# Kernel tuning notes

Hardware: AMD Instinct MI355X
Metric: run time of the kernel (lower is better)

The kernel has to match this reference:

```python
import jax, jax.numpy as jnp
import numpy as np

V, D, B, L = 100000, 64, 4096, 200

def setup_inputs() -> dict:
    key = jax.random.key(0)
    ks = jax.random.split(key, 10)
    s = 0.05  # keep activations in a sane range for sigmoid
    return {
        "item_ids": jax.random.randint(ks[0], (B,), 0, V),
        "history": jax.random.randint(ks[1], (B, L), 0, V),
        "hist_len": jax.random.randint(ks[2], (B,), 1, L + 1),
        "emb_table": jax.random.normal(ks[3], (V, D), jnp.float32) * s,
        "aW1": jax.random.normal(ks[4], (3 * D, D), jnp.float32) * s,
        "ab1": jnp.zeros((D,), jnp.float32),
        "aW2": jax.random.normal(ks[5], (D, 1), jnp.float32) * s,
        "ab2": jnp.zeros((1,), jnp.float32),
        "fW1": jax.random.normal(ks[6], (3 * D, 128), jnp.float32) * s,
        "fb1": jnp.zeros((128,), jnp.float32),
        "fW2": jax.random.normal(ks[7], (128, 64), jnp.float32) * s,
        "fb2": jnp.zeros((64,), jnp.float32),
        "fW3": jax.random.normal(ks[8], (64, 1), jnp.float32) * s,
        "fb3": jnp.zeros((1,), jnp.float32),
    }

def reference(item_ids, history, hist_len, emb_table, aW1, ab1, aW2, ab2,
              fW1, fb1, fW2, fb2, fW3, fb3):
    target = emb_table[item_ids]                      # [B, D]
    hist = emb_table[history]                         # [B, L, D]
    # original pads short histories with zero rows -> zero the padded tail
    mask = (jnp.arange(hist.shape[1])[None, :] < hist_len[:, None]).astype(hist.dtype)
    hist = hist * mask[..., None]
    tgt = jnp.broadcast_to(target[:, None, :], hist.shape)     # [B, L, D]
    # attention_fc takes 3*D features: (hist, target, hist*target)
    feat = jnp.concatenate([hist, tgt, hist * tgt], axis=-1)   # [B, L, 3D]
    h = jax.nn.relu(feat @ aW1 + ab1)                 # [B, L, D]
    scores = (h @ aW2 + ab2)[..., 0]                  # [B, L]
    # faithful to original: softmax over full padded length (no length mask)
    w = jax.nn.softmax(scores, axis=1)
    pooled = jnp.einsum('bl,bld->bd', w, hist)        # [B, D]
    comb = jnp.concatenate([target, pooled, pooled - target], axis=-1)  # [B, 3D]
    z = jax.nn.relu(comb @ fW1 + fb1)
    z = jax.nn.relu(z @ fW2 + fb2)
    return jax.nn.sigmoid(z @ fW3 + fb3)              # [B, 1]
```

## Files before the change

kernel.cpp:

```cpp
#include <hip/hip_runtime.h>
#include <hip/hip_bf16.h>

#define NV 100000
#define ND 64
#define NB 4096
#define NL 200
#define MT 13

typedef __bf16 bf16_t;
typedef __bf16 bf16x8 __attribute__((ext_vector_type(8)));
typedef float f32x4 __attribute__((ext_vector_type(4)));

#define TB_ELEMS ((long)NV * ND)
#define FW1_ELEMS (192 * 128)
#define FW2_ELEMS (128 * 64)
#define CVT_TOTAL (TB_ELEMS + FW1_ELEMS + FW2_ELEMS)

__global__ __launch_bounds__(256)
void cvt_kernel(const float* __restrict__ emb,
                const float* __restrict__ fW1,
                const float* __restrict__ fW2,
                bf16_t* __restrict__ tb)
{
    long i = ((long)blockIdx.x * 256 + threadIdx.x) * 8;
    if (i >= CVT_TOTAL) return;
    const float* src;
    if (i < TB_ELEMS)                  src = emb + i;
    else if (i < TB_ELEMS + FW1_ELEMS) src = fW1 + (i - TB_ELEMS);
    else                               src = fW2 + (i - TB_ELEMS - FW1_ELEMS);
    f32x4 a0 = *(const f32x4*)(src);
    f32x4 a1 = *(const f32x4*)(src + 4);
    bf16x8 o;
#pragma unroll
    for (int j = 0; j < 4; ++j) { o[j] = (bf16_t)a0[j]; o[j + 4] = (bf16_t)a1[j]; }
    *(bf16x8*)(tb + i) = o;
}

__global__ __launch_bounds__(512, 4)
void din_kernel1(const int* __restrict__ item_ids,
                 const int* __restrict__ history,
                 const int* __restrict__ hist_len,
                 const float* __restrict__ emb,
                 const bf16_t* __restrict__ tb,
                 const float* __restrict__ aW1,
                 const float* __restrict__ ab1,
                 const float* __restrict__ aW2,
                 const bf16_t* __restrict__ fW1b, const float* __restrict__ fb1,
                 const bf16_t* __restrict__ fW2b, const float* __restrict__ fb2,
                 const float* __restrict__ fW3, const float* __restrict__ fb3,
                 float* __restrict__ out)
{
    __shared__ __align__(16) bf16_t histA[2][208 * 64];
    __shared__ __align__(16) bf16_t wbT[2][64 * 64];
    __shared__ float tgt[2][64];
    __shared__ __align__(16) float scores[2][208];
    __shared__ float wts[2][208];
    __shared__ float pp2[2][512];
    __shared__ float red[2][8];

    float* pp7 = (float*)histA;
    float* z1  = (float*)histA + 8192;
    float* z2  = (float*)histA + 8448;

    const int b0  = blockIdx.x * 2;
    const int tid = threadIdx.x;
    const int len0 = hist_len[b0];
    const int len1 = hist_len[b0 + 1];

    if (tid < 128) {
        int bx = tid >> 6, d = tid & 63;
        tgt[bx][d] = emb[(long)item_ids[b0 + bx] * ND + d];
    }

    {
        const int p = tid & 1;
        const int s = tid >> 1;
        const int bxA = (s >= 208);
        const int lA  = s - bxA * 208;
        const int lB  = s + 48;
        const int lenA = bxA ? len1 : len0;
        const bool vB = (s < 160);
        const bf16x8 z = (bf16x8)(bf16_t)0.f;
        bf16x8 a0 = z, a1 = z, a2 = z, a3 = z;
        bf16x8 c0 = z, c1 = z, c2 = z, c3 = z;
        if (lA < lenA) {
            const bf16_t* src = tb + (long)history[(long)(b0 + bxA) * NL + lA] * ND + p * 32;
            a0 = *(const bf16x8*)(src);
            a1 = *(const bf16x8*)(src + 8);
            a2 = *(const bf16x8*)(src + 16);
            a3 = *(const bf16x8*)(src + 24);
        }
        if (vB && lB < len1) {
            const bf16_t* src = tb + (long)history[(long)(b0 + 1) * NL + lB] * ND + p * 32;
            c0 = *(const bf16x8*)(src);
            c1 = *(const bf16x8*)(src + 8);
            c2 = *(const bf16x8*)(src + 16);
            c3 = *(const bf16x8*)(src + 24);
        }
        {
            bf16_t* d = &histA[bxA][lA * 64];
            const int S = (lA & 7) << 3;
            *(bf16x8*)&d[(p * 32 +  0) ^ S] = a0;
            *(bf16x8*)&d[(p * 32 +  8) ^ S] = a1;
            *(bf16x8*)&d[(p * 32 + 16) ^ S] = a2;
            *(bf16x8*)&d[(p * 32 + 24) ^ S] = a3;
        }
        if (vB) {
            bf16_t* d = &histA[1][lB * 64];
            const int S = (lB & 7) << 3;
            *(bf16x8*)&d[(p * 32 +  0) ^ S] = c0;
            *(bf16x8*)&d[(p * 32 +  8) ^ S] = c1;
            *(bf16x8*)&d[(p * 32 + 16) ^ S] = c2;
            *(bf16x8*)&d[(p * 32 + 24) ^ S] = c3;
        }
    }

    {
        const int n  = tid & 63;
        const int kp = tid >> 6;
        const long t0 = (long)item_ids[b0] * ND;
        const long t1 = (long)item_ids[b0 + 1] * ND;
        f32x4 tk0a = *(const f32x4*)(emb + t0 + kp * 8);
        f32x4 tk0b = *(const f32x4*)(emb + t0 + kp * 8 + 4);
        f32x4 tk1a = *(const f32x4*)(emb + t1 + kp * 8);
        f32x4 tk1b = *(const f32x4*)(emb + t1 + kp * 8 + 4);
        float cs0 = 0.f, cs1 = 0.f;
        bf16x8 w0v, w1v;
#pragma unroll
        for (int i = 0; i < 8; ++i) {
            int k = kp * 8 + i;
            float tk0 = (i < 4) ? tk0a[i] : tk0b[i - 4];
            float tk1 = (i < 4) ? tk1a[i] : tk1b[i - 4];
            float ah = aW1[k * 64 + n];
            float am = aW1[(64 + k) * 64 + n];
            float ap = aW1[(128 + k) * 64 + n];
            w0v[i] = (bf16_t)(ah + tk0 * ap);
            w1v[i] = (bf16_t)(ah + tk1 * ap);
            cs0 += tk0 * am;
            cs1 += tk1 * am;
        }
        const int S = (n & 7) << 3;
        *(bf16x8*)&wbT[0][n * 64 + ((kp * 8) ^ S)] = w0v;
        *(bf16x8*)&wbT[1][n * 64 + ((kp * 8) ^ S)] = w1v;
        pp2[0][kp * 64 + n] = cs0;
        pp2[1][kp * 64 + n] = cs1;
    }
    __syncthreads();

    {
        const int wave = tid >> 6;
        const int lane = tid & 63;
        const int bx   = wave & 1;
        const int col  = lane & 15;
        const int quad = lane >> 4;

        bf16x8 bfrag[4][2];
#pragma unroll
        for (int nt = 0; nt < 4; ++nt) {
            const int n = nt * 16 + col;
            const int S = (n & 7) << 3;
#pragma unroll
            for (int kb = 0; kb < 2; ++kb)
                bfrag[nt][kb] = *(const bf16x8*)&wbT[bx][n * 64 + ((kb * 32 + quad * 8) ^ S)];
        }
        float cvals[4], a2vals[4];
#pragma unroll
        for (int nt = 0; nt < 4; ++nt) {
            const int n = nt * 16 + col;
            float s = ab1[n];
#pragma unroll
            for (int kp = 0; kp < 8; ++kp) s += pp2[bx][kp * 64 + n];
            cvals[nt]  = s;
            a2vals[nt] = aW2[n];
        }

        for (int mt = (wave >> 1); mt < MT; mt += 4) {
            const int row = mt * 16 + col;
            const int S   = (row & 7) << 3;
            const bf16_t* base = &histA[bx][row * 64];
            bf16x8 af0 = *(const bf16x8*)&base[(     quad * 8) ^ S];
            bf16x8 af1 = *(const bf16x8*)&base[(32 + quad * 8) ^ S];
            float sc[4] = {0.f, 0.f, 0.f, 0.f};
#pragma unroll
            for (int nt = 0; nt < 4; ++nt) {
                f32x4 acc = {0.f, 0.f, 0.f, 0.f};
                acc = __builtin_amdgcn_mfma_f32_16x16x32_bf16(af0, bfrag[nt][0], acc, 0, 0, 0);
                acc = __builtin_amdgcn_mfma_f32_16x16x32_bf16(af1, bfrag[nt][1], acc, 0, 0, 0);
#pragma unroll
                for (int i = 0; i < 4; ++i) {
                    float h = acc[i] + cvals[nt];
                    h = h > 0.f ? h : 0.f;
                    sc[i] += h * a2vals[nt];
                }
            }
            for (int off = 1; off < 16; off <<= 1)
#pragma unroll
                for (int i = 0; i < 4; ++i)
                    sc[i] += __shfl_xor(sc[i], off, 64);
            if (col == 0) {
                f32x4 outv = {sc[0], sc[1], sc[2], sc[3]};
                *(f32x4*)&scores[bx][mt * 16 + quad * 4] = outv;
            }
        }
    }
    __syncthreads();

    {
        const int bx = tid >> 8, t = tid & 255;
        float s = (t < NL) ? scores[bx][t] : -1e30f;
        float m = s;
        for (int off = 32; off > 0; off >>= 1) m = fmaxf(m, __shfl_xor(m, off, 64));
        if ((t & 63) == 0) red[bx][t >> 6] = m;
        __syncthreads();
        m = fmaxf(fmaxf(red[bx][0], red[bx][1]), fmaxf(red[bx][2], red[bx][3]));
        float e = (t < NL) ? __expf(s - m) : 0.f;
        if (t < NL) wts[bx][t] = e;
        float ss = e;
        for (int off = 32; off > 0; off >>= 1) ss += __shfl_xor(ss, off, 64);
        if ((t & 63) == 0) red[bx][4 + (t >> 6)] = ss;
        __syncthreads();
    }

    {
        const int wave = tid >> 6, lane = tid & 63;
        const int bx = wave >> 2, q = wave & 3;
        const float rtot = 1.f / (red[bx][4] + red[bx][5] + red[bx][6] + red[bx][7]);
        float acc = 0.f;
        for (int i = 0; i < 50; ++i) {
            int l = q * 50 + i;
            acc += wts[bx][l] * (float)histA[bx][l * 64 + (lane ^ ((l & 7) << 3))];
        }
        pp2[bx][q * 64 + lane] = acc * rtot;
    }
    __syncthreads();

    {
        const int bx = tid >> 8, t = tid & 255;
        if (t < 192) {
            const int d = t & 63;
            float v;
            if (t < 64) v = tgt[bx][d];
            else {
                float pl = pp2[bx][d] + pp2[bx][64 + d] + pp2[bx][128 + d] + pp2[bx][192 + d];
                v = (t < 128) ? pl : pl - tgt[bx][d];
            }
            scores[bx][t] = v;
        }
    }
    __syncthreads();

    {
        const int cg = tid & 15;
        const int g  = tid >> 4;
        f32x4 a00 = {0,0,0,0}, a01 = {0,0,0,0};
        f32x4 a10 = {0,0,0,0}, a11 = {0,0,0,0};
#pragma unroll
        for (int ii = 0; ii < 6; ++ii) {
            int i = g * 6 + ii;
            bf16x8 wv = *(const bf16x8*)&fW1b[i * 128 + cg * 8];
            float c0 = scores[0][i], c1 = scores[1][i];
#pragma unroll
            for (int jj = 0; jj < 4; ++jj) {
                float wA = (float)wv[jj], wB = (float)wv[4 + jj];
                a00[jj] += c0 * wA;  a01[jj] += c0 * wB;
                a10[jj] += c1 * wA;  a11[jj] += c1 * wB;
            }
        }
        *(f32x4*)&pp7[g * 256 +       cg * 8    ] = a00;
        *(f32x4*)&pp7[g * 256 +       cg * 8 + 4] = a01;
        *(f32x4*)&pp7[g * 256 + 128 + cg * 8    ] = a10;
        *(f32x4*)&pp7[g * 256 + 128 + cg * 8 + 4] = a11;
    }
    __syncthreads();
    if (tid < 256) {
        const int bx = tid >> 7, j = tid & 127;
        float s = fb1[j];
#pragma unroll
        for (int g = 0; g < 32; ++g) s += pp7[g * 256 + bx * 128 + j];
        z1[bx * 128 + j] = fmaxf(s, 0.f);
    }
    __syncthreads();

    {
        const int cg = tid & 7;
        const int g  = tid >> 3;
        f32x4 a00 = {0,0,0,0}, a01 = {0,0,0,0};
        f32x4 a10 = {0,0,0,0}, a11 = {0,0,0,0};
#pragma unroll
        for (int ii = 0; ii < 2; ++ii) {
            int i = g * 2 + ii;
            bf16x8 wv = *(const bf16x8*)&fW2b[i * 64 + cg * 8];
            float v0 = z1[i], v1 = z1[128 + i];
#pragma unroll
            for (int jj = 0; jj < 4; ++jj) {
                float wA = (float)wv[jj], wB = (float)wv[4 + jj];
                a00[jj] += v0 * wA;  a01[jj] += v0 * wB;
                a10[jj] += v1 * wA;  a11[jj] += v1 * wB;
            }
        }
        *(f32x4*)&pp7[g * 128 +      cg * 8    ] = a00;
        *(f32x4*)&pp7[g * 128 +      cg * 8 + 4] = a01;
        *(f32x4*)&pp7[g * 128 + 64 + cg * 8    ] = a10;
        *(f32x4*)&pp7[g * 128 + 64 + cg * 8 + 4] = a11;
    }
    __syncthreads();
    if (tid < 128) {
        const int bx = tid >> 6, j = tid & 63;
        float s = fb2[j];
#pragma unroll
        for (int g = 0; g < 64; ++g) s += pp7[g * 128 + bx * 64 + j];
        z2[bx * 64 + j] = fmaxf(s, 0.f);
    }
    __syncthreads();

    if (tid < 128) {
        const int bx = tid >> 6, j = tid & 63;
        float s = z2[bx * 64 + j] * fW3[j];
        for (int off = 32; off > 0; off >>= 1) s += __shfl_xor(s, off, 64);
        if (j == 0) out[b0 + bx] = 1.f / (1.f + __expf(-(s + fb3[0])));
    }
}

extern "C" void kernel_launch(void* const* d_in, const int* in_sizes, int n_in,
                              void* d_out, int out_size, void* d_ws, size_t ws_size,
                              hipStream_t stream) {
    const int*   item_ids = (const int*)d_in[0];
    const int*   history  = (const int*)d_in[1];
    const int*   hist_len = (const int*)d_in[2];
    const float* emb      = (const float*)d_in[3];
    const float* aW1      = (const float*)d_in[4];
    const float* ab1      = (const float*)d_in[5];
    const float* aW2      = (const float*)d_in[6];
    const float* fW1      = (const float*)d_in[8];
    const float* fb1      = (const float*)d_in[9];
    const float* fW2      = (const float*)d_in[10];
    const float* fb2      = (const float*)d_in[11];
    const float* fW3      = (const float*)d_in[12];
    const float* fb3      = (const float*)d_in[13];

    bf16_t* tb   = (bf16_t*)d_ws;
    bf16_t* fW1b = tb + TB_ELEMS;
    bf16_t* fW2b = fW1b + FW1_ELEMS;

    cvt_kernel<<<(int)((CVT_TOTAL / 8 + 255) / 256), 256, 0, stream>>>(emb, fW1, fW2, tb);
    din_kernel1<<<NB / 2, 512, 0, stream>>>(item_ids, history, hist_len, emb, tb,
                                            aW1, ab1, aW2,
                                            fW1b, fb1, fW2b, fb2, fW3, fb3,
                                            (float*)d_out);
}
```

Before: 149.1 us.

## Move final MLP layers onto MFMA with transposed bf16 weights and swap attention operands

The convert kernel now writes fW1 and fW2 transposed as bf16. The two final MLP layers use 16x16x32 MFMA instructions with batch rows padded to 16, replacing the scalar partial-sum reductions through shared memory and removing several barriers. The attention score MFMA swaps operands so each lane holds a history row's partial score, cutting the shuffle reduction to two steps. Weighted pooling is restructured into vectorized bf16x4 loads with shuffle reduction. The risk is that most of the padded MFMA work is wasted, since only 2 of 16 rows are real, and the layout changes add shared memory aliasing complexity.

```diff
diff --git a/kernel.cpp b/kernel.cpp
--- a/kernel.cpp
+++ b/kernel.cpp
@@ -9,31 +9,44 @@
 
 typedef __bf16 bf16_t;
 typedef __bf16 bf16x8 __attribute__((ext_vector_type(8)));
+typedef __bf16 bf16x4 __attribute__((ext_vector_type(4)));
 typedef float f32x4 __attribute__((ext_vector_type(4)));
 
 #define TB_ELEMS ((long)NV * ND)
-#define FW1_ELEMS (192 * 128)
-#define FW2_ELEMS (128 * 64)
-#define CVT_TOTAL (TB_ELEMS + FW1_ELEMS + FW2_ELEMS)
+#define TBV (TB_ELEMS / 8)
+#define FT1 (128 * 192)
+#define FT2 (64 * 128)
+#define CVT_TASKS (TBV + FT1 + FT2)
 
 __global__ __launch_bounds__(256)
 void cvt_kernel(const float* __restrict__ emb,
                 const float* __restrict__ fW1,
                 const float* __restrict__ fW2,
-                bf16_t* __restrict__ tb)
+                bf16_t* __restrict__ tb,
+                bf16_t* __restrict__ fW1T,
+                bf16_t* __restrict__ fW2T)
 {
-    long i = ((long)blockIdx.x * 256 + threadIdx.x) * 8;
-    if (i >= CVT_TOTAL) return;
-    const float* src;
-    if (i < TB_ELEMS)                  src = emb + i;
-    else if (i < TB_ELEMS + FW1_ELEMS) src = fW1 + (i - TB_ELEMS);
-    else                               src = fW2 + (i - TB_ELEMS - FW1_ELEMS);
-    f32x4 a0 = *(const f32x4*)(src);
-    f32x4 a1 = *(const f32x4*)(src + 4);
-    bf16x8 o;
-#pragma unroll
-    for (int j = 0; j < 4; ++j) { o[j] = (bf16_t)a0[j]; o[j + 4] = (bf16_t)a1[j]; }
-    *(bf16x8*)(tb + i) = o;
+    long t = (long)blockIdx.x * 256 + threadIdx.x;
+    if (t >= CVT_TASKS) return;
+    if (t < TBV) {
+        long i = t * 8;
+        f32x4 a0 = *(const f32x4*)(emb + i);
+        f32x4 a1 = *(const f32x4*)(emb + i + 4);
+        bf16x8 o;
+#pragma unroll
+        for (int j = 0; j < 4; ++j) { o[j] = (bf16_t)a0[j]; o[j + 4] = (bf16_t)a1[j]; }
+        *(bf16x8*)(tb + i) = o;
+    } else {
+        int u = (int)(t - TBV);
+        if (u < FT1) {
+            int n = u / 192, k = u - n * 192;
+            fW1T[u] = (bf16_t)fW1[k * 128 + n];
+        } else {
+            int u2 = u - FT1;
+            int n = u2 >> 7, k = u2 & 127;
+            fW2T[u2] = (bf16_t)fW2[k * 64 + n];
+        }
+    }
 }
 
 __global__ __launch_bounds__(512, 4)
@@ -45,8 +58,8 @@
                  const float* __restrict__ aW1,
                  const float* __restrict__ ab1,
                  const float* __restrict__ aW2,
-                 const bf16_t* __restrict__ fW1b, const float* __restrict__ fb1,
-                 const bf16_t* __restrict__ fW2b, const float* __restrict__ fb2,
+                 const bf16_t* __restrict__ fW1T, const float* __restrict__ fb1,
+                 const bf16_t* __restrict__ fW2T, const float* __restrict__ fb2,
                  const float* __restrict__ fW3, const float* __restrict__ fb3,
                  float* __restrict__ out)
 {
@@ -57,10 +70,11 @@
     __shared__ float wts[2][208];
     __shared__ float pp2[2][512];
     __shared__ float red[2][8];
-
-    float* pp7 = (float*)histA;
-    float* z1  = (float*)histA + 8192;
-    float* z2  = (float*)histA + 8448;
+    __shared__ float cb2[2][64];
+
+    bf16_t* comb16 = (bf16_t*)wbT;
+    bf16_t* z1s    = (bf16_t*)wbT + 3200;
+    float*  z2f    = (float*)((bf16_t*)wbT + 5376);
 
     const int b0  = blockIdx.x * 2;
     const int tid = threadIdx.x;
@@ -147,6 +161,15 @@
     }
     __syncthreads();
 
+    if (tid < 128) {
+        const int bx = tid >> 6, n = tid & 63;
+        float s = ab1[n];
+#pragma unroll
+        for (int kp = 0; kp < 8; ++kp) s += pp2[bx][kp * 64 + n];
+        cb2[bx][n] = s;
+    }
+    __syncthreads();
+
     {
         const int wave = tid >> 6;
         const int lane = tid & 63;
@@ -154,53 +177,47 @@
         const int col  = lane & 15;
         const int quad = lane >> 4;
 
-        bf16x8 bfrag[4][2];
+        bf16x8 afrag[4][2];
 #pragma unroll
         for (int nt = 0; nt < 4; ++nt) {
             const int n = nt * 16 + col;
             const int S = (n & 7) << 3;
 #pragma unroll
             for (int kb = 0; kb < 2; ++kb)
-                bfrag[nt][kb] = *(const bf16x8*)&wbT[bx][n * 64 + ((kb * 32 + quad * 8) ^ S)];
-        }
-        float cvals[4], a2vals[4];
-#pragma unroll
-        for (int nt = 0; nt < 4; ++nt) {
-            const int n = nt * 16 + col;
-            float s = ab1[n];
-#pragma unroll
-            for (int kp = 0; kp < 8; ++kp) s += pp2[bx][kp * 64 + n];
-            cvals[nt]  = s;
-            a2vals[nt] = aW2[n];
-        }
+                afrag[nt][kb] = *(const bf16x8*)&wbT[bx][n * 64 + ((kb * 32 + quad * 8) ^ S)];
+        }
+        float cv[4][4], a2[4][4];
+#pragma unroll
+        for (int nt = 0; nt < 4; ++nt)
+#pragma unroll
+            for (int i = 0; i < 4; ++i) {
+                const int no = nt * 16 + quad * 4 + i;
+                cv[nt][i] = cb2[bx][no];
+                a2[nt][i] = aW2[no];
+            }
 
         for (int mt = (wave >> 1); mt < MT; mt += 4) {
-            const int row = mt * 16 + col;
-            const int S   = (row & 7) << 3;
-            const bf16_t* base = &histA[bx][row * 64];
-            bf16x8 af0 = *(const bf16x8*)&base[(     quad * 8) ^ S];
-            bf16x8 af1 = *(const bf16x8*)&base[(32 + quad * 8) ^ S];
-            float sc[4] = {0.f, 0.f, 0.f, 0.f};
+            const int l = mt * 16 + col;
+            const int S = (l & 7) << 3;
+            const bf16_t* base = &histA[bx][l * 64];
+            bf16x8 bf0 = *(const bf16x8*)&base[(     quad * 8) ^ S];
+            bf16x8 bf1 = *(const bf16x8*)&base[(32 + quad * 8) ^ S];
+            float sc = 0.f;
 #pragma unroll
             for (int nt = 0; nt < 4; ++nt) {
                 f32x4 acc = {0.f, 0.f, 0.f, 0.f};
-                acc = __builtin_amdgcn_mfma_f32_16x16x32_bf16(af0, bfrag[nt][0], acc, 0, 0, 0);
-                acc = __builtin_amdgcn_mfma_f32_16x16x32_bf16(af1, bfrag[nt][1], acc, 0, 0, 0);
+                acc = __builtin_amdgcn_mfma_f32_16x16x32_bf16(afrag[nt][0], bf0, acc, 0, 0, 0);
+                acc = __builtin_amdgcn_mfma_f32_16x16x32_bf16(afrag[nt][1], bf1, acc, 0, 0, 0);
 #pragma unroll
                 for (int i = 0; i < 4; ++i) {
-                    float h = acc[i] + cvals[nt];
+                    float h = acc[i] + cv[nt][i];
                     h = h > 0.f ? h : 0.f;
-                    sc[i] += h * a2vals[nt];
+                    sc += h * a2[nt][i];
                 }
             }
-            for (int off = 1; off < 16; off <<= 1)
-#pragma unroll
-                for (int i = 0; i < 4; ++i)
-                    sc[i] += __shfl_xor(sc[i], off, 64);
-            if (col == 0) {
-                f32x4 outv = {sc[0], sc[1], sc[2], sc[3]};
-                *(f32x4*)&scores[bx][mt * 16 + quad * 4] = outv;
-            }
+            sc += __shfl_xor(sc, 16, 64);
+            sc += __shfl_xor(sc, 32, 64);
+            if (quad == 0) scores[bx][mt * 16 + col] = sc;
         }
     }
     __syncthreads();
@@ -215,6 +232,7 @@
         m = fmaxf(fmaxf(red[bx][0], red[bx][1]), fmaxf(red[bx][2], red[bx][3]));
         float e = (t < NL) ? __expf(s - m) : 0.f;
         if (t < NL) wts[bx][t] = e;
+        else if (t < 208) wts[bx][t] = 0.f;
         float ss = e;
         for (int off = 32; off > 0; off >>= 1) ss += __shfl_xor(ss, off, 64);
         if ((t & 63) == 0) red[bx][4 + (t >> 6)] = ss;
@@ -222,15 +240,46 @@
     }
 
     {
+        const int bx = tid >> 8, t = tid & 255;
+        const int c = t & 15;
+        const int g = t >> 4;
+        const int w4 = (tid >> 6) & 3;
+        const float rtot = 1.f / (red[bx][4] + red[bx][5] + red[bx][6] + red[bx][7]);
+        f32x4 acc = {0.f, 0.f, 0.f, 0.f};
+#pragma unroll
+        for (int j = 0; j < 13; ++j) {
+            const int l = g + j * 16;
+            const float wl = wts[bx][l];
+            bf16x4 v = *(const bf16x4*)&histA[bx][l * 64 + ((c * 4) ^ ((l & 7) << 3))];
+#pragma unroll
+            for (int k = 0; k < 4; ++k) acc[k] += wl * (float)v[k];
+        }
+#pragma unroll
+        for (int k = 0; k < 4; ++k) {
+            acc[k] += __shfl_xor(acc[k], 16, 64);
+            acc[k] += __shfl_xor(acc[k], 32, 64);
+            acc[k] *= rtot;
+        }
+        if ((tid & 63) < 16) *(f32x4*)&pp2[bx][w4 * 64 + c * 4] = acc;
+    }
+
+    bf16x8 bw1[6]; float b1v;
+    bf16x8 bw2[4]; float b2v = 0.f;
+    {
         const int wave = tid >> 6, lane = tid & 63;
-        const int bx = wave >> 2, q = wave & 3;
-        const float rtot = 1.f / (red[bx][4] + red[bx][5] + red[bx][6] + red[bx][7]);
-        float acc = 0.f;
-        for (int i = 0; i < 50; ++i) {
-            int l = q * 50 + i;
-            acc += wts[bx][l] * (float)histA[bx][l * 64 + (lane ^ ((l & 7) << 3))];
-        }
-        pp2[bx][q * 64 + lane] = acc * rtot;
+        const int col = lane & 15, quad = lane >> 4;
+        const int n = wave * 16 + col;
+#pragma unroll
+        for (int ks = 0; ks < 6; ++ks)
+            bw1[ks] = *(const bf16x8*)&fW1T[(long)n * 192 + ks * 32 + quad * 8];
+        b1v = fb1[n];
+        if (wave < 4) {
+            const int n2 = wave * 16 + col;
+#pragma unroll
+            for (int ks = 0; ks < 4; ++ks)
+                bw2[ks] = *(const bf16x8*)&fW2T[(long)n2 * 128 + ks * 32 + quad * 8];
+            b2v = fb2[n2];
+        }
     }
     __syncthreads();
 
@@ -244,78 +293,59 @@
                 float pl = pp2[bx][d] + pp2[bx][64 + d] + pp2[bx][128 + d] + pp2[bx][192 + d];
                 v = (t < 128) ? pl : pl - tgt[bx][d];
             }
-            scores[bx][t] = v;
-        }
-    }
-    __syncthreads();
-
-    {
-        const int cg = tid & 15;
-        const int g  = tid >> 4;
-        f32x4 a00 = {0,0,0,0}, a01 = {0,0,0,0};
-        f32x4 a10 = {0,0,0,0}, a11 = {0,0,0,0};
-#pragma unroll
-        for (int ii = 0; ii < 6; ++ii) {
-            int i = g * 6 + ii;
-            bf16x8 wv = *(const bf16x8*)&fW1b[i * 128 + cg * 8];
-            float c0 = scores[0][i], c1 = scores[1][i];
-#pragma unroll
-            for (int jj = 0; jj < 4; ++jj) {
-                float wA = (float)wv[jj], wB = (float)wv[4 + jj];
-                a00[jj] += c0 * wA;  a01[jj] += c0 * wB;
-                a10[jj] += c1 * wA;  a11[jj] += c1 * wB;
-            }
-        }
-        *(f32x4*)&pp7[g * 256 +       cg * 8    ] = a00;
-        *(f32x4*)&pp7[g * 256 +       cg * 8 + 4] = a01;
-        *(f32x4*)&pp7[g * 256 + 128 + cg * 8    ] = a10;
-        *(f32x4*)&pp7[g * 256 + 128 + cg * 8 + 4] = a11;
-    }
-    __syncthreads();
-    if (tid < 256) {
-        const int bx = tid >> 7, j = tid & 127;
-        float s = fb1[j];
-#pragma unroll
-        for (int g = 0; g < 32; ++g) s += pp7[g * 256 + bx * 128 + j];
-        z1[bx * 128 + j] = fmaxf(s, 0.f);
-    }
-    __syncthreads();
-
-    {
-        const int cg = tid & 7;
-        const int g  = tid >> 3;
-        f32x4 a00 = {0,0,0,0}, a01 = {0,0,0,0};
-        f32x4 a10 = {0,0,0,0}, a11 = {0,0,0,0};
-#pragma unroll
-        for (int ii = 0; ii < 2; ++ii) {
-            int i = g * 2 + ii;
-            bf16x8 wv = *(const bf16x8*)&fW2b[i * 64 + cg * 8];
-            float v0 = z1[i], v1 = z1[128 + i];
-#pragma unroll
-            for (int jj = 0; jj < 4; ++jj) {
-                float wA = (float)wv[jj], wB = (float)wv[4 + jj];
-                a00[jj] += v0 * wA;  a01[jj] += v0 * wB;
-                a10[jj] += v1 * wA;  a11[jj] += v1 * wB;
-            }
-        }
-        *(f32x4*)&pp7[g * 128 +      cg * 8    ] = a00;
-        *(f32x4*)&pp7[g * 128 +      cg * 8 + 4] = a01;
-        *(f32x4*)&pp7[g * 128 + 64 + cg * 8    ] = a10;
-        *(f32x4*)&pp7[g * 128 + 64 + cg * 8 + 4] = a11;
-    }
-    __syncthreads();
+            comb16[bx * 200 + t] = (bf16_t)v;
+        }
+        if (tid >= 384) {
+            const bf16x8 z = (bf16x8)(bf16_t)0.f;
+            const int u = tid - 384;
+#pragma unroll
+            for (int s = u; s < 350; s += 128) *(bf16x8*)&comb16[400 + s * 8] = z;
+        }
+    }
+    __syncthreads();
+
+    {
+        const int wave = tid >> 6, lane = tid & 63;
+        const int col = lane & 15, quad = lane >> 4;
+        f32x4 acc = {0.f, 0.f, 0.f, 0.f};
+#pragma unroll
+        for (int ks = 0; ks < 6; ++ks) {
+            bf16x8 a = *(const bf16x8*)&comb16[col * 200 + ks * 32 + quad * 8];
+            acc = __builtin_amdgcn_mfma_f32_16x16x32_bf16(a, bw1[ks], acc, 0, 0, 0);
+        }
+        const int n = wave * 16 + col;
+#pragma unroll
+        for (int i = 0; i < 4; ++i) {
+            const int m = quad * 4 + i;
+            float zv = (m < 2) ? fmaxf(acc[i] + b1v, 0.f) : 0.f;
+            z1s[m * 136 + n] = (bf16_t)zv;
+        }
+    }
+    __syncthreads();
+
+    {
+        const int wave = tid >> 6, lane = tid & 63;
+        const int col = lane & 15, quad = lane >> 4;
+        if (wave < 4) {
+            f32x4 acc = {0.f, 0.f, 0.f, 0.f};
+#pragma unroll
+            for (int ks = 0; ks < 4; ++ks) {
+                bf16x8 a = *(const bf16x8*)&z1s[col * 136 + ks * 32 + quad * 8];
+                acc = __builtin_amdgcn_mfma_f32_16x16x32_bf16(a, bw2[ks], acc, 0, 0, 0);
+            }
+            const int n2 = wave * 16 + col;
+#pragma unroll
+            for (int i = 0; i < 4; ++i) {
+                const int m = quad * 4 + i;
+                if (m < 2) z2f[m * 64 + n2] = fmaxf(acc[i] + b2v, 0.f);
+            }
+        }
+    }
+    __syncthreads();
+
     if (tid < 128) {
         const int bx = tid >> 6, j = tid & 63;
-        float s = fb2[j];
-#pragma unroll
-        for (int g = 0; g < 64; ++g) s += pp7[g * 128 + bx * 64 + j];
-        z2[bx * 64 + j] = fmaxf(s, 0.f);
-    }
-    __syncthreads();
-
-    if (tid < 128) {
-        const int bx = tid >> 6, j = tid & 63;
-        float s = z2[bx * 64 + j] * fW3[j];
+        float s = z2f[bx * 64 + j] * fW3[j];
         for (int off = 32; off > 0; off >>= 1) s += __shfl_xor(s, off, 64);
         if (j == 0) out[b0 + bx] = 1.f / (1.f + __expf(-(s + fb3[0])));
     }
@@ -339,12 +369,13 @@
     const float* fb3      = (const float*)d_in[13];
 
     bf16_t* tb   = (bf16_t*)d_ws;
-    bf16_t* fW1b = tb + TB_ELEMS;
-    bf16_t* fW2b = fW1b + FW1_ELEMS;
-
-    cvt_kernel<<<(int)((CVT_TOTAL / 8 + 255) / 256), 256, 0, stream>>>(emb, fW1, fW2, tb);
+    bf16_t* fW1T = tb + TB_ELEMS;
+    bf16_t* fW2T = fW1T + FT1;
+
+    cvt_kernel<<<(int)((CVT_TASKS + 255) / 256), 256, 0, stream>>>(emb, fW1, fW2,
+                                                                   tb, fW1T, fW2T);
     din_kernel1<<<NB / 2, 512, 0, stream>>>(item_ids, history, hist_len, emb, tb,
                                             aW1, ab1, aW2,
-                                            fW1b, fb1, fW2b, fb2, fW3, fb3,
+                                            fW1T, fb1, fW2T, fb2, fW3, fb3,
                                             (float*)d_out);
 }
```

New measurement: 140.1 us. -6.1%, faster.
